# Kernel optimization log

Hardware: AMD Instinct MI355X
Metric: run time of the kernel (lower is better)

## Reference

```python
import jax, jax.numpy as jnp
import numpy as np

B, N, E = 64, 512, 524288
DA, DE, DH, DR, DI = 70, 14, 200, 16, 6
T_SCALE = float(np.sqrt(1.0 / 200.0))
D_MIN, D_MAX, D_COUNT = 0.0, 5.0, 16


def _layernorm(x, g, b, eps=1e-5):
    m = jnp.mean(x, axis=-1, keepdims=True)
    v = jnp.var(x, axis=-1, keepdims=True)
    return g * (x - m) * jax.lax.rsqrt(v + eps) + b


def setup_inputs() -> dict:
    key = jax.random.key(0)
    ks = jax.random.split(key, 24)
    d = {
        'atom_feat1': jax.random.normal(ks[0], (B, N, DA), jnp.float32),
        'atom_feat2': jax.random.normal(ks[1], (B, N, DA), jnp.float32),
        'coords1': jax.random.normal(ks[2], (B, N, 3), jnp.float32) * 3.0,
        'coords2': jax.random.normal(ks[3], (B, N, 3), jnp.float32) * 3.0,
        'edge_feat1': jax.random.normal(ks[4], (E, DE), jnp.float32),
        'edge_feat2': jax.random.normal(ks[5], (E, DE), jnp.float32),
        'interaction1': jax.random.normal(ks[6], (B, N, DI), jnp.float32),
        'interaction2': jax.random.normal(ks[7], (B, N, DI), jnp.float32),
        'edge_src1': jax.random.randint(ks[8], (E,), 0, B * N, jnp.int32),
        'edge_dst1': jax.random.randint(ks[9], (E,), 0, B * N, jnp.int32),
        'edge_src2': jax.random.randint(ks[10], (E,), 0, B * N, jnp.int32),
        'edge_dst2': jax.random.randint(ks[11], (E,), 0, B * N, jnp.int32),
        # parameters (scaled for stability)
        'W_atom': jax.random.normal(ks[12], (DA, DH), jnp.float32) * 0.1,
        'W_edge': jax.random.normal(ks[13], (DE, 100), jnp.float32) * 0.1,
        'W_rbf': jax.random.normal(ks[14], (D_COUNT, 100), jnp.float32) * 0.1,
        'b_rbf': jnp.zeros((100,), jnp.float32),
        'ln_g': jnp.ones((DH,), jnp.float32),
        'ln_b': jnp.zeros((DH,), jnp.float32),
        'W_down': jax.random.normal(ks[15], (2 * DH, DH), jnp.float32) * 0.05,
        'degree_table': jax.random.normal(ks[16], (200, DH), jnp.float32).at[0].set(0.0) * 0.1,
        'W_f1': jax.random.normal(ks[17], (3 * (DH + DI), 400), jnp.float32) * 0.05,
        'b_f1': jnp.zeros((400,), jnp.float32),
        'W_f2': jax.random.normal(ks[18], (400, 200), jnp.float32) * 0.05,
        'b_f2': jnp.zeros((200,), jnp.float32),
        'W_f3': jax.random.normal(ks[19], (200, 100), jnp.float32) * 0.05,
        'b_f3': jnp.zeros((100,), jnp.float32),
        'W_f4': jax.random.normal(ks[20], (100, 1), jnp.float32) * 0.05,
        'b_f4': jnp.zeros((1,), jnp.float32),
    }
    return d


def _side(atom, coords, efeat, src, dst, W_atom, W_edge, W_rbf, b_rbf, ln_g, ln_b):
    # atom: [B,N,DA], coords: [B,N,3], efeat: [E,DE], src/dst: [E] flat node ids
    BN = B * N
    h = jax.nn.relu(jnp.einsum('bna,ad->bnd', atom, W_atom)).reshape(BN, DH)
    e = jax.nn.relu(efeat @ W_edge)                      # [E,100]
    cflat = coords.reshape(BN, 3)
    diff = cflat[src] - cflat[dst]                       # [E,3]
    dist = jnp.sqrt(jnp.sum(diff * diff, axis=-1) + 1e-12)
    mu = jnp.linspace(D_MIN, D_MAX, D_COUNT)             # [16]
    sigma = (D_MAX - D_MIN) / D_COUNT
    rbf = jnp.exp(-(((dist[:, None] - mu[None, :]) / sigma) ** 2))  # [E,16]
    r = jax.nn.relu(rbf @ W_rbf + b_rbf)                 # [E,100]
    eh = jnp.concatenate([e, r], axis=-1)                # [E,200]
    h = _layernorm(h, ln_g, ln_b)
    eh = _layernorm(eh, ln_g, ln_b)
    # one message-passing aggregation (encoder step): scatter edge msgs to dst
    h = h + jax.ops.segment_sum(eh, dst, num_segments=BN)
    deg = jax.ops.segment_sum(jnp.ones((E,), jnp.int32), dst, num_segments=BN)
    deg = jnp.clip(deg, 0, 199)                          # in_degrees -> embedding idx
    return h.reshape(B, N, DH), deg.reshape(B, N)


def reference(atom_feat1, atom_feat2, coords1, coords2, edge_feat1, edge_feat2,
              interaction1, interaction2, edge_src1, edge_dst1, edge_src2, edge_dst2,
              W_atom, W_edge, W_rbf, b_rbf, ln_g, ln_b, W_down, degree_table,
              W_f1, b_f1, W_f2, b_f2, W_f3, b_f3, W_f4, b_f4):
    h1, d1 = _side(atom_feat1, coords1, edge_feat1, edge_src1, edge_dst1,
                   W_atom, W_edge, W_rbf, b_rbf, ln_g, ln_b)
    h2, d2 = _side(atom_feat2, coords2, edge_feat2, edge_src2, edge_dst2,
                   W_atom, W_edge, W_rbf, b_rbf, ln_g, ln_b)
    # batched cross-attention (atom_cross_att), vectorized over B
    att = jnp.einsum('bnd,bmd->bnm', h1, h2) * T_SCALE   # [B,N,N]
    a2 = jax.nn.softmax(att, axis=-1)
    a1 = jax.nn.softmax(att, axis=-2)
    c1 = jnp.einsum('bnm,bmd->bnd', a2, h2)              # for_hg1
    c2 = jnp.einsum('bnm,bnd->bmd', a1, h1)              # for_hg2
    h1 = jax.nn.relu(jnp.einsum('bnk,kd->bnd', jnp.concatenate([h1, c1], -1), W_down))
    h2 = jax.nn.relu(jnp.einsum('bnk,kd->bnd', jnp.concatenate([h2, c2], -1), W_down))
    h1 = h1 + degree_table[d1]
    h2 = h2 + degree_table[d2]
    # readout: mean over nodes, concat mean interaction embedding
    hsg1 = jnp.concatenate([jnp.mean(h1, axis=1), jnp.mean(interaction1, axis=1)], -1)
    hsg2 = jnp.concatenate([jnp.mean(h2, axis=1), jnp.mean(interaction2, axis=1)], -1)
    x = jnp.concatenate([hsg1, hsg2, hsg1 - hsg2], axis=-1)  # [B, 3*(200+6)]
    x = jax.nn.relu(x @ W_f1 + b_f1)
    x = jax.nn.relu(x @ W_f2 + b_f2)
    x = jax.nn.relu(x @ W_f3 + b_f3)
    zk = x @ W_f4 + b_f4                                 # [B,1]
    return zk
```

## Files before the change

kernel.cpp:

```cpp
#include <hip/hip_runtime.h>
#include <cstddef>
#include <cstdint>

#define BB   64
#define NN   512
#define BN   (BB*NN)
#define HBN  16384
#define EE   524288
#define DA   70
#define DE   14
#define DH   200
#define DI   6
#define T_SCALE 0.07071067811865475f

typedef __attribute__((ext_vector_type(8))) short short8;
typedef __attribute__((ext_vector_type(4))) float f32x4;

__device__ __forceinline__ short f2bf(float x) {
    union { float f; unsigned u; } v; v.f = x;
    const unsigned r = v.u + 0x7FFFu + ((v.u >> 16) & 1u);
    return (short)(r >> 16);
}
__device__ __forceinline__ float bf2f(short s) {
    union { unsigned u; float f; } v;
    v.u = ((unsigned)(unsigned short)s) << 16;
    return v.f;
}

__device__ __forceinline__ float dpp16_sum(float x) {
    union { float f; int i; } a, b;
    a.f = x;
    b.i = __builtin_amdgcn_update_dpp(0, a.i, 0xB1, 0xF, 0xF, false); a.f += b.f;
    b.i = __builtin_amdgcn_update_dpp(0, a.i, 0x4E, 0xF, 0xF, false); a.f += b.f;
    b.i = __builtin_amdgcn_update_dpp(0, a.i, 0x141, 0xF, 0xF, false); a.f += b.f;
    b.i = __builtin_amdgcn_update_dpp(0, a.i, 0x140, 0xF, 0xF, false); a.f += b.f;
    return a.f;
}

__global__ __launch_bounds__(256) void prologue_kernel(
    const float* __restrict__ atom1, const float* __restrict__ atom2,
    const float* __restrict__ W_atom,
    const float* __restrict__ ln_g, const float* __restrict__ ln_b,
    float* __restrict__ h1, float* __restrict__ h2,
    const int* __restrict__ edst1, const int* __restrict__ edst2,
    int* __restrict__ deg1, int* __restrict__ deg2,
    int* __restrict__ rank1, int* __restrict__ rank2,
    const float* __restrict__ W_edge, const float* __restrict__ W_rbf,
    const float* __restrict__ b_rbf,
    short* __restrict__ WTH, short* __restrict__ WTL,
    short* __restrict__ featH1, short* __restrict__ featH2,
    const float* __restrict__ W_down,
    short* __restrict__ WbTH, short* __restrict__ WbTL)
{
    const int bid = blockIdx.x;
    const int tid = threadIdx.x;

    if (bid < 4096) {
        const int side = bid >> 11;
        const float* atom = side ? atom2 : atom1;
        float* h = side ? h2 : h1;
        const int node0 = (bid & 2047) * 16;

        __shared__ float arow[16][DA];
        __shared__ float vals[16][DH];

        for (int i = tid; i < 16*DA; i += 256) {
            const int n = i / DA, k = i % DA;
            arow[n][k] = atom[(size_t)(node0+n)*DA + k];
        }
        __syncthreads();

        if (tid < DH) {
            float a[16];
            #pragma unroll
            for (int n = 0; n < 16; n++) a[n] = 0.f;
            for (int k = 0; k < DA; k++) {
                const float w = W_atom[k*DH + tid];
                #pragma unroll
                for (int n = 0; n < 16; n++) a[n] += arow[n][k]*w;
            }
            #pragma unroll
            for (int n = 0; n < 16; n++) vals[n][tid] = fmaxf(a[n], 0.f);
        }
        __syncthreads();

        const int wv = tid >> 6, lane = tid & 63;
        #pragma unroll 1
        for (int rr = 0; rr < 4; rr++) {
            const int n = rr*4 + wv;
            float v0 = vals[n][lane];
            float v1 = vals[n][64+lane];
            float v2 = vals[n][128+lane];
            float v3 = (lane < 8) ? vals[n][192+lane] : 0.0f;
            float s  = v0+v1+v2+v3;
            float s2 = v0*v0+v1*v1+v2*v2+v3*v3;
            #pragma unroll
            for (int off = 1; off < 64; off <<= 1) {
                s  += __shfl_xor(s,  off, 64);
                s2 += __shfl_xor(s2, off, 64);
            }
            const float mean = s * (1.0f/DH);
            const float var  = s2 * (1.0f/DH) - mean*mean;
            const float rstd = rsqrtf(var + 1e-5f);
            const size_t base = (size_t)(node0+n)*DH;
            h[base + lane]       = ln_g[lane]     *(v0-mean)*rstd + ln_b[lane];
            h[base + 64 + lane]  = ln_g[64+lane]  *(v1-mean)*rstd + ln_b[64+lane];
            h[base + 128 + lane] = ln_g[128+lane] *(v2-mean)*rstd + ln_b[128+lane];
            if (lane < 8)
                h[base + 192 + lane] = ln_g[192+lane]*(v3-mean)*rstd + ln_b[192+lane];
        }
        return;
    }

    if (bid < 6144) {
        const int e = (bid - 4096)*256 + tid;
        rank1[e] = atomicAdd(&deg1[edst1[e]], 1);
        rank2[e] = atomicAdd(&deg2[edst2[e]], 1);
        return;
    }

    if (bid < 6508) {
        const int idx = (bid - 6144)*256 + tid;
        if (idx >= 208*448) return;
        const int c = idx / 448, kk = idx - c*448;
        float v = 0.f;
        if (c < 200) {
            if (kk < 200) v = W_down[(size_t)kk*DH + c];
            else if (kk >= 224 && kk < 424) v = W_down[(size_t)(200 + kk - 224)*DH + c];
        }
        const short hi = f2bf(v);
        WbTH[idx] = hi;
        WbTL[idx] = f2bf(v - bf2f(hi));
        return;
    }

    {
        const int pb = bid - 6508;
        if (pb >= 26) {
            short* f = (pb == 26) ? featH1 : featH2;
            f[(size_t)EE*32 + tid] = 0;
            f[(size_t)EE*32 + 256 + tid] = 0;
            return;
        }
        const int idx = pb*256 + tid;
        const int c = idx >> 5, k = idx & 31;
        float v = 0.f;
        if (c < 100) {
            if (k < 14) v = W_edge[k*100 + c];
        } else if (c < 200) {
            const int cc = c - 100;
            if (k >= 14 && k < 30) v = W_rbf[(k-14)*100 + cc];
            else if (k == 30) v = b_rbf[cc];
        }
        const short hi = f2bf(v);
        WTH[idx] = hi;
        WTL[idx] = f2bf(v - bf2f(hi));
    }
}

__global__ __launch_bounds__(1024) void scan_kernel(
    const int* __restrict__ deg1, const int* __restrict__ deg2,
    int* __restrict__ start1, int* __restrict__ start2)
{
    const int side = blockIdx.x;
    const int* deg   = side ? deg2 : deg1;
    int* start  = side ? start2 : start1;

    __shared__ int part[1024];
    const int t = threadIdx.x;
    const int base = t * 32;
    int local[32];
    int sum = 0;
    #pragma unroll
    for (int i = 0; i < 8; i++) {
        const int4 v = *(const int4*)&deg[base + i*4];
        local[4*i+0] = v.x; local[4*i+1] = v.y;
        local[4*i+2] = v.z; local[4*i+3] = v.w;
        sum += v.x + v.y + v.z + v.w;
    }
    part[t] = sum;
    __syncthreads();
    for (int off = 1; off < 1024; off <<= 1) {
        int v = (t >= off) ? part[t-off] : 0;
        __syncthreads();
        part[t] += v;
        __syncthreads();
    }
    int run = part[t] - sum;
    #pragma unroll
    for (int i = 0; i < 32; i++) {
        start[base+i] = run;
        run += local[i];
    }
    if (t == 1023) start[BN] = run;
}

__global__ __launch_bounds__(256) void featgen_kernel(
    const float* __restrict__ efeat1, const float* __restrict__ efeat2,
    const int* __restrict__ esrc1, const int* __restrict__ esrc2,
    const int* __restrict__ edst1, const int* __restrict__ edst2,
    const float* __restrict__ coords1, const float* __restrict__ coords2,
    const int* __restrict__ rank1, const int* __restrict__ rank2,
    const int* __restrict__ start1, const int* __restrict__ start2,
    short* __restrict__ featH1, short* __restrict__ featH2)
{
    const int side = blockIdx.y;
    const float* ef     = side ? efeat2  : efeat1;
    const int*   esrc   = side ? esrc2   : esrc1;
    const int*   edst   = side ? edst2   : edst1;
    const float* coords = side ? coords2 : coords1;
    const int*   rank   = side ? rank2   : rank1;
    const int*   start  = side ? start2  : start1;
    short* featH = side ? featH2 : featH1;

    const int e = blockIdx.x*256 + threadIdx.x;
    const int src = esrc[e], dst = edst[e];

    short f[32];
    #pragma unroll
    for (int k = 0; k < 14; k++) f[k] = f2bf(ef[(size_t)e*DE + k]);

    const float dx = coords[src*3+0] - coords[dst*3+0];
    const float dy = coords[src*3+1] - coords[dst*3+1];
    const float dz = coords[src*3+2] - coords[dst*3+2];
    const float dist = sqrtf(dx*dx + dy*dy + dz*dz + 1e-12f);
    #pragma unroll
    for (int k = 0; k < 16; k++) {
        const float t = 3.2f*dist - 1.0666666667f*(float)k;
        f[14+k] = f2bf(__expf(-t*t));
    }
    f[30] = f2bf(1.0f);
    f[31] = 0;

    const int slot = start[dst] + rank[e];
    short* out = featH + (size_t)slot*32;
    #pragma unroll
    for (int q = 0; q < 4; q++)
        *(short8*)&out[q*8] = *(short8*)&f[q*8];
}

__global__ __launch_bounds__(256, 2) void gather_mfma(
    const short* __restrict__ featH1, const short* __restrict__ featH2,
    const int* __restrict__ start1, const int* __restrict__ start2,
    const short* __restrict__ WTH, const short* __restrict__ WTL,
    const float* __restrict__ ln_g, const float* __restrict__ ln_b,
    float* __restrict__ h1, float* __restrict__ h2)
{
    __shared__ short sWH[208*40];
    __shared__ short sWL[208*40];
    __shared__ float plane[4][216];

    const int tid = threadIdx.x;
    const int wv = tid >> 6, lane = tid & 63;
    const int arow = lane & 15, aq = lane >> 4;

    for (int f = tid; f < 832; f += 256) {
        const int d = f >> 2, cc = (f & 3) * 8;
        *(short8*)&sWH[d*40 + cc] = *(const short8*)&WTH[f*8];
        *(short8*)&sWL[d*40 + cc] = *(const short8*)&WTL[f*8];
    }
    __syncthreads();

    const int side = blockIdx.y;
    const short* feat = side ? featH2 : featH1;
    const int*  start = side ? start2 : start1;
    float* h = side ? h2 : h1;

    const int c0 = blockIdx.x*16 + wv*4;

    const float g0 = ln_g[lane],      bb0 = ln_b[lane];
    const float g1 = ln_g[64+lane],   bb1 = ln_b[64+lane];
    const float g2 = ln_g[128+lane],  bb2 = ln_b[128+lane];
    const float g3 = (lane < 8) ? ln_g[192+lane] : 0.f;
    const float bb3 = (lane < 8) ? ln_b[192+lane] : 0.f;

    const int sidx = (lane < 5) ? lane : 4;
    const int sv = start[c0 + sidx];

    const int lb = arow*40 + aq*8;

    #pragma unroll 1
    for (int ni = 0; ni < 4; ni++) {
        const int st = __builtin_amdgcn_readlane(sv, ni);
        const int en = __builtin_amdgcn_readlane(sv, ni + 1);
        const int dg = en - st;
        const int node = c0 + ni;
        const size_t hbase = (size_t)node * DH;

        const float hv0 = h[hbase + lane];
        const float hv1 = h[hbase + 64 + lane];
        const float hv2 = h[hbase + 128 + lane];
        const float hv3 = (lane < 8) ? h[hbase + 192 + lane] : 0.f;

        float colacc[13];
        #pragma unroll
        for (int nt = 0; nt < 13; nt++) colacc[nt] = 0.f;
        float musum = 0.f;

        short8 aC = *(const short8*)&feat[(size_t)(st + arow)*32 + aq*8];

        for (int t0 = 0; t0 < dg; t0 += 16) {
            const short8 aN = *(const short8*)&feat[(size_t)(st + t0 + 16 + arow)*32 + aq*8];

            f32x4 acc[13];
            #pragma unroll
            for (int nt = 0; nt < 13; nt++) {
                const short8 whv = *(const short8*)&sWH[nt*640 + lb];
                const short8 wlv = *(const short8*)&sWL[nt*640 + lb];
                f32x4 z = (f32x4){0.f,0.f,0.f,0.f};
                z = __builtin_amdgcn_mfma_f32_16x16x32_bf16(aC, whv, z, 0, 0, 0);
                z = __builtin_amdgcn_mfma_f32_16x16x32_bf16(aC, wlv, z, 0, 0, 0);
                acc[nt] = z;
            }
            float sr[4] = {0.f,0.f,0.f,0.f}, s2r[4] = {0.f,0.f,0.f,0.f};
            #pragma unroll
            for (int nt = 0; nt < 13; nt++) {
                #pragma unroll
                for (int r = 0; r < 4; r++) {
                    const float v = fmaxf(acc[nt][r], 0.f);
                    acc[nt][r] = v;
                    sr[r] += v; s2r[r] += v*v;
                }
            }
            #pragma unroll
            for (int r = 0; r < 4; r++) {
                sr[r]  = dpp16_sum(sr[r]);
                s2r[r] = dpp16_sum(s2r[r]);
            }
            #pragma unroll
            for (int r = 0; r < 4; r++) {
                const bool valid = (t0 + aq*4 + r) < dg;
                const float mean = sr[r] * (1.0f/DH);
                const float var  = s2r[r] * (1.0f/DH) - mean*mean;
                const float rs   = rsqrtf(var + 1e-5f);
                const float rstd = valid ? rs : 0.f;
                musum += valid ? mean*rs : 0.f;
                #pragma unroll
                for (int nt = 0; nt < 13; nt++)
                    colacc[nt] += rstd*acc[nt][r];
            }
            aC = aN;
        }

        #pragma unroll
        for (int nt = 0; nt < 13; nt++) {
            colacc[nt] += __shfl_xor(colacc[nt], 16, 64);
            colacc[nt] += __shfl_xor(colacc[nt], 32, 64);
        }
        musum += __shfl_xor(musum, 16, 64);
        musum += __shfl_xor(musum, 32, 64);

        if (aq == 0) {
            #pragma unroll
            for (int nt = 0; nt < 13; nt++)
                plane[wv][nt*16 + arow] = colacc[nt];
        }

        const float dgf = (float)dg;
        h[hbase + lane]       = hv0 + g0*(plane[wv][lane]     - musum) + dgf*bb0;
        h[hbase + 64 + lane]  = hv1 + g1*(plane[wv][64+lane]  - musum) + dgf*bb1;
        h[hbase + 128 + lane] = hv2 + g2*(plane[wv][128+lane] - musum) + dgf*bb2;
        if (lane < 8)
            h[hbase + 192 + lane] = hv3 + g3*(plane[wv][192+lane] - musum) + dgf*bb3;
    }
}

__global__ __launch_bounds__(256) void cvt_kernel(
    const float* __restrict__ h1, const float* __restrict__ h2, const int half,
    short* __restrict__ hbH1, short* __restrict__ hbL1,
    short* __restrict__ hbH2, short* __restrict__ hbL2,
    short* __restrict__ hTH1, short* __restrict__ hTL1,
    short* __restrict__ hTH2, short* __restrict__ hTL2)
{
    const int side = blockIdx.y;
    const float* h = side ? h2 : h1;
    short* hbH = side ? hbH2 : hbH1;
    short* hbL = side ? hbL2 : hbL1;
    short* hTH = side ? hTH2 : hTH1;
    short* hTL = side ? hTL2 : hTL1;

    const int nl0 = blockIdx.x * 64;
    const int bl = nl0 >> 9, m0 = nl0 & 511;
    const int ng0 = half*HBN + nl0;

    __shared__ short tH[64][226];
    __shared__ short tL[64][226];
    const int tid = threadIdx.x;
    for (int i = tid; i < 64*224; i += 256) {
        const int r = i / 224, c = i - r*224;
        const float v = (c < DH) ? h[(size_t)(ng0+r)*DH + c] : 0.f;
        const short hi = f2bf(v);
        const short lo = f2bf(v - bf2f(hi));
        tH[r][c] = hi; tL[r][c] = lo;
        hbH[(size_t)(nl0+r)*224 + c] = hi;
        hbL[(size_t)(nl0+r)*224 + c] = lo;
    }
    __syncthreads();
    for (int i = tid; i < 224*64; i += 256) {
        const int c = i >> 6, m = i & 63;
        const size_t o = ((size_t)bl*224 + c)*NN + m0 + m;
        hTH[o] = tH[m][c];
        hTL[o] = tL[m][c];
    }
}

__global__ __launch_bounds__(512, 2) void attn_kernel(
    const short* __restrict__ hbH1, const short* __restrict__ hbL1,
    const short* __restrict__ hbH2, const short* __restrict__ hbL2,
    const short* __restrict__ hTH1, const short* __restrict__ hTL1,
    const short* __restrict__ hTH2, const short* __restrict__ hTL2,
    short* __restrict__ cb1, short* __restrict__ cb2)
{
    const int id  = blockIdx.x;
    const int xcd = id & 7, m = id >> 3;
    const int r   = m >> 6;
    const int b01 = (m >> 5) & 1;
    const int dir = (m >> 4) & 1;
    const int qb  = m & 15;
    const int b   = xcd*4 + r*2 + b01;
    const int q0  = qb << 5;

    const short *Qh, *Ql, *Kh, *Kl, *Vh, *Vl;
    short* cb;
    if (dir == 0) {
        Qh = hbH1 + (size_t)b*NN*224;  Ql = hbL1 + (size_t)b*NN*224;
        Kh = hbH2 + (size_t)b*NN*224;  Kl = hbL2 + (size_t)b*NN*224;
        Vh = hTH2 + (size_t)b*224*NN;  Vl = hTL2 + (size_t)b*224*NN;
        cb = cb1;
    } else {
        Qh = hbH2 + (size_t)b*NN*224;  Ql = hbL2 + (size_t)b*NN*224;
        Kh = hbH1 + (size_t)b*NN*224;  Kl = hbL1 + (size_t)b*NN*224;
        Vh = hTH1 + (size_t)b*224*NN;  Vl = hTL1 + (size_t)b*224*NN;
        cb = cb2;
    }

    __shared__ short smem[32*520];
    short* sQh = smem;
    short* sQl = smem + 7424;
    short* pb  = smem;
    __shared__ float sm_[8][32];
    __shared__ float ss_[8][32];

    const int tid = threadIdx.x;
    const int wv = tid >> 6, lane = tid & 63;
    const int arow = lane & 15, aq = lane >> 4;

    for (int i = tid; i < 896; i += 512) {
        const int rr = i / 28, c = (i - rr*28) * 8;
        *(short8*)&sQh[rr*232 + c] = *(const short8*)&Qh[(size_t)(q0 + rr)*224 + c];
        *(short8*)&sQl[rr*232 + c] = *(const short8*)&Ql[(size_t)(q0 + rr)*224 + c];
    }
    __syncthreads();

    f32x4 acc[2][4];
    #pragma unroll
    for (int g = 0; g < 2; g++)
        #pragma unroll
        for (int t = 0; t < 4; t++) acc[g][t] = (f32x4){0.f,0.f,0.f,0.f};

    const int qb_off = arow*232 + aq*8;
    #pragma unroll 1
    for (int k = 0; k < 7; k++) {
        const short8 qh0 = *(const short8*)&sQh[qb_off + k*32];
        const short8 ql0 = *(const short8*)&sQl[qb_off + k*32];
        const short8 qh1 = *(const short8*)&sQh[qb_off + 16*232 + k*32];
        const short8 ql1 = *(const short8*)&sQl[qb_off + 16*232 + k*32];
        #pragma unroll
        for (int t = 0; t < 4; t++) {
            const size_t kb = (size_t)((wv*4 + t)*16 + arow)*224 + k*32 + aq*8;
            const short8 bh = *(const short8*)&Kh[kb];
            const short8 bl = *(const short8*)&Kl[kb];
            acc[0][t] = __builtin_amdgcn_mfma_f32_16x16x32_bf16(qh0, bh, acc[0][t], 0, 0, 0);
            acc[0][t] = __builtin_amdgcn_mfma_f32_16x16x32_bf16(qh0, bl, acc[0][t], 0, 0, 0);
            acc[0][t] = __builtin_amdgcn_mfma_f32_16x16x32_bf16(ql0, bh, acc[0][t], 0, 0, 0);
            acc[1][t] = __builtin_amdgcn_mfma_f32_16x16x32_bf16(qh1, bh, acc[1][t], 0, 0, 0);
            acc[1][t] = __builtin_amdgcn_mfma_f32_16x16x32_bf16(qh1, bl, acc[1][t], 0, 0, 0);
            acc[1][t] = __builtin_amdgcn_mfma_f32_16x16x32_bf16(ql1, bh, acc[1][t], 0, 0, 0);
        }
    }

    float iv[2][4];
    #pragma unroll
    for (int g = 0; g < 2; g++) {
        #pragma unroll
        for (int r2 = 0; r2 < 4; r2++) {
            float mx = -1e30f;
            #pragma unroll
            for (int t = 0; t < 4; t++) {
                acc[g][t][r2] *= T_SCALE;
                mx = fmaxf(mx, acc[g][t][r2]);
            }
            mx = fmaxf(mx, __shfl_xor(mx, 1, 64));
            mx = fmaxf(mx, __shfl_xor(mx, 2, 64));
            mx = fmaxf(mx, __shfl_xor(mx, 4, 64));
            mx = fmaxf(mx, __shfl_xor(mx, 8, 64));
            if (arow == 0) sm_[wv][g*16 + aq*4 + r2] = mx;
        }
    }
    __syncthreads();
    #pragma unroll
    for (int g = 0; g < 2; g++) {
        #pragma unroll
        for (int r2 = 0; r2 < 4; r2++) {
            const int row = g*16 + aq*4 + r2;
            float M = sm_[0][row];
            #pragma unroll
            for (int w = 1; w < 8; w++) M = fmaxf(M, sm_[w][row]);
            float s = 0.f;
            #pragma unroll
            for (int t = 0; t < 4; t++) {
                const float e = __expf(acc[g][t][r2] - M);
                acc[g][t][r2] = e;
                s += e;
            }
            s += __shfl_xor(s, 1, 64);
            s += __shfl_xor(s, 2, 64);
            s += __shfl_xor(s, 4, 64);
            s += __shfl_xor(s, 8, 64);
            if (arow == 0) ss_[wv][row] = s;
        }
    }
    __syncthreads();
    #pragma unroll
    for (int g = 0; g < 2; g++) {
        #pragma unroll
        for (int r2 = 0; r2 < 4; r2++) {
            const int row = g*16 + aq*4 + r2;
            float s = ss_[0][row];
            #pragma unroll
            for (int w = 1; w < 8; w++) s += ss_[w][row];
            iv[g][r2] = 1.0f / s;
        }
    }
    #pragma unroll
    for (int g = 0; g < 2; g++) {
        #pragma unroll
        for (int t = 0; t < 4; t++) {
            const int col = (wv*4 + t)*16 + arow;
            #pragma unroll
            for (int r2 = 0; r2 < 4; r2++)
                pb[(g*16 + aq*4 + r2)*520 + col] = f2bf(acc[g][t][r2] * iv[g][r2]);
        }
    }
    __syncthreads();

    const int nbase = (wv < 5) ? 2*wv : 10 + (wv - 5);
    const int ncnt  = (wv < 5) ? 2 : 1;
    f32x4 pacc[2][2];
    #pragma unroll
    for (int g = 0; g < 2; g++)
        #pragma unroll
        for (int t = 0; t < 2; t++) pacc[g][t] = (f32x4){0.f,0.f,0.f,0.f};

    for (int k0 = 0; k0 < NN; k0 += 32) {
        const short8 a0 = *(const short8*)&pb[arow*520 + k0 + aq*8];
        const short8 a1 = *(const short8*)&pb[(16 + arow)*520 + k0 + aq*8];
        #pragma unroll
        for (int t = 0; t < 2; t++) {
            if (t < ncnt) {
                const size_t vb = (size_t)((nbase+t)*16 + arow)*NN + k0 + aq*8;
                const short8 bh = *(const short8*)&Vh[vb];
                const short8 bl = *(const short8*)&Vl[vb];
                pacc[0][t] = __builtin_amdgcn_mfma_f32_16x16x32_bf16(a0, bh, pacc[0][t], 0, 0, 0);
                pacc[0][t] = __builtin_amdgcn_mfma_f32_16x16x32_bf16(a0, bl, pacc[0][t], 0, 0, 0);
                pacc[1][t] = __builtin_amdgcn_mfma_f32_16x16x32_bf16(a1, bh, pacc[1][t], 0, 0, 0);
                pacc[1][t] = __builtin_amdgcn_mfma_f32_16x16x32_bf16(a1, bl, pacc[1][t], 0, 0, 0);
            }
        }
    }

    #pragma unroll
    for (int t = 0; t < 2; t++) {
        if (t < ncnt) {
            const int col = (nbase+t)*16 + arow;
            #pragma unroll
            for (int g = 0; g < 2; g++) {
                #pragma unroll
                for (int r2 = 0; r2 < 4; r2++) {
                    const int row = q0 + g*16 + aq*4 + r2;
                    const short v = (col < DH) ? f2bf(pacc[g][t][r2]) : (short)0;
                    cb[((size_t)b*NN + row)*224 + col] = v;
                }
            }
        }
    }
    if (wv == 7) {
        const int col = 208 + arow;
        #pragma unroll
        for (int g = 0; g < 2; g++) {
            #pragma unroll
            for (int r2 = 0; r2 < 4; r2++) {
                const int row = q0 + g*16 + aq*4 + r2;
                cb[((size_t)b*NN + row)*224 + col] = 0;
            }
        }
    }
}

__global__ __launch_bounds__(512, 2) void down_mfma(
    const short* __restrict__ hbH1, const short* __restrict__ hbH2,
    const short* __restrict__ cb1, const short* __restrict__ cb2,
    const int* __restrict__ deg1, const int* __restrict__ deg2,
    const short* __restrict__ WbTH, const short* __restrict__ WbTL,
    const float* __restrict__ degree_table,
    float* __restrict__ hsg1, float* __restrict__ hsg2, const int half)
{
    const int side = blockIdx.y;
    const short* X0 = side ? hbH2 : hbH1;
    const short* X1 = side ? cb2 : cb1;
    const int*   dgp = side ? deg2 : deg1;
    float* hsg = side ? hsg2 : hsg1;

    const int nl0 = blockIdx.x * 128;
    const int ng0 = half*HBN + nl0;
    const int b = ng0 >> 9;

    __shared__ short As[128*40];
    __shared__ short BsH[208*40];
    __shared__ short BsL[208*40];
    __shared__ float part[208];

    const int tid = threadIdx.x;
    const int wv = tid >> 6, lane = tid & 63;
    const int arow = lane & 15, aq = lane >> 4;

    if (tid < 208) part[tid] = 0.f;

    f32x4 acc[13];
    #pragma unroll
    for (int t = 0; t < 13; t++) acc[t] = (f32x4){0.f,0.f,0.f,0.f};

    const int sr = tid >> 2, sc = (tid & 3) * 8;

    for (int phase = 0; phase < 2; phase++) {
        const short* X = phase ? X1 : X0;
        for (int k0 = 0; k0 < 224; k0 += 32) {
            __syncthreads();
            *(short8*)&As[sr*40 + sc] =
                *(const short8*)&X[(size_t)(nl0+sr)*224 + k0 + sc];
            const int kkg = phase*224 + k0;
            #pragma unroll
            for (int pass = 0; pass < 2; pass++) {
                const int f = pass*512 + tid;
                if (f < 832) {
                    const int d = f >> 2, cc = (f & 3) * 8;
                    *(short8*)&BsH[d*40 + cc] = *(const short8*)&WbTH[(size_t)d*448 + kkg + cc];
                    *(short8*)&BsL[d*40 + cc] = *(const short8*)&WbTL[(size_t)d*448 + kkg + cc];
                }
            }
            __syncthreads();
            const short8 a = *(const short8*)&As[(16*wv + arow)*40 + aq*8];
            #pragma unroll
            for (int t = 0; t < 13; t++) {
                const short8 bh = *(const short8*)&BsH[(t*16 + arow)*40 + aq*8];
                const short8 bl = *(const short8*)&BsL[(t*16 + arow)*40 + aq*8];
                acc[t] = __builtin_amdgcn_mfma_f32_16x16x32_bf16(a, bh, acc[t], 0, 0, 0);
                acc[t] = __builtin_amdgcn_mfma_f32_16x16x32_bf16(a, bl, acc[t], 0, 0, 0);
            }
        }
    }
    __syncthreads();

    int dgc[4];
    #pragma unroll
    for (int r = 0; r < 4; r++) {
        int d = dgp[ng0 + 16*wv + aq*4 + r];
        dgc[r] = d > 199 ? 199 : d;
    }
    #pragma unroll
    for (int nt = 0; nt < 13; nt++) {
        const int col = nt*16 + arow;
        float s = 0.f;
        if (col < DH) {
            #pragma unroll
            for (int r = 0; r < 4; r++)
                s += fmaxf(acc[nt][r], 0.f) + degree_table[dgc[r]*DH + col];
        }
        s += __shfl_xor(s, 16, 64);
        s += __shfl_xor(s, 32, 64);
        if (lane < 16 && col < DH) atomicAdd(&part[col], s);
    }
    __syncthreads();
    if (tid < DH) unsafeAtomicAdd(&hsg[b*206 + tid], part[tid] * (1.0f/512.0f));
}

__global__ __launch_bounds__(256) void mlp_kernel(
    const float* __restrict__ hsg1, const float* __restrict__ hsg2,
    const float* __restrict__ i1, const float* __restrict__ i2,
    const float* __restrict__ W_f1, const float* __restrict__ b_f1,
    const float* __restrict__ W_f2, const float* __restrict__ b_f2,
    const float* __restrict__ W_f3, const float* __restrict__ b_f3,
    const float* __restrict__ W_f4, const float* __restrict__ b_f4,
    float* __restrict__ out)
{
    const int b = blockIdx.x;
    __shared__ float x[618];
    __shared__ float y1[400];
    __shared__ float y2[200];
    __shared__ float y3[100];
    __shared__ float red[256];
    const int tid = threadIdx.x;

    if (tid < 192) {
        const int j = tid % 6, seg = tid / 6;
        float s1 = 0.f, s2 = 0.f;
        for (int n = seg*16; n < seg*16 + 16; n++) {
            s1 += i1[(size_t)b*NN*DI + n*DI + j];
            s2 += i2[(size_t)b*NN*DI + n*DI + j];
        }
        red[tid] = s1;
        y2[tid] = s2;
    }
    __syncthreads();
    if (tid < 206) {
        float a, bb;
        if (tid < 200) {
            a = hsg1[b*206 + tid]; bb = hsg2[b*206 + tid];
        } else {
            const int j = tid - 200;
            float t1 = 0.f, t2 = 0.f;
            for (int sg = 0; sg < 32; sg++) { t1 += red[sg*6 + j]; t2 += y2[sg*6 + j]; }
            a = t1 * (1.0f/512.0f); bb = t2 * (1.0f/512.0f);
        }
        x[tid] = a; x[206 + tid] = bb; x[412 + tid] = a - bb;
    }
    __syncthreads();
    for (int c = tid; c < 400; c += 256) {
        float acc = b_f1[c];
        for (int k = 0; k < 618; k++) acc += x[k]*W_f1[(size_t)k*400 + c];
        y1[c] = fmaxf(acc, 0.0f);
    }
    __syncthreads();
    if (tid < 200) {
        float acc = b_f2[tid];
        for (int k = 0; k < 400; k++) acc += y1[k]*W_f2[k*200 + tid];
        y2[tid] = fmaxf(acc, 0.0f);
    }
    __syncthreads();
    if (tid < 100) {
        float acc = b_f3[tid];
        for (int k = 0; k < 200; k++) acc += y2[k]*W_f3[k*100 + tid];
        y3[tid] = fmaxf(acc, 0.0f);
    }
    __syncthreads();
    red[tid] = (tid < 100) ? y3[tid]*W_f4[tid] : 0.0f;
    __syncthreads();
    for (int s = 128; s > 0; s >>= 1) {
        if (tid < s) red[tid] += red[tid + s];
        __syncthreads();
    }
    if (tid == 0) out[b] = red[0] + b_f4[0];
}

extern "C" void kernel_launch(void* const* d_in, const int* in_sizes, int n_in,
                              void* d_out, int out_size, void* d_ws, size_t ws_size,
                              hipStream_t stream)
{
    const float* atom1  = (const float*)d_in[0];
    const float* atom2  = (const float*)d_in[1];
    const float* coords1= (const float*)d_in[2];
    const float* coords2= (const float*)d_in[3];
    const float* efeat1 = (const float*)d_in[4];
    const float* efeat2 = (const float*)d_in[5];
    const float* inter1 = (const float*)d_in[6];
    const float* inter2 = (const float*)d_in[7];
    const int*   esrc1  = (const int*)d_in[8];
    const int*   edst1  = (const int*)d_in[9];
    const int*   esrc2  = (const int*)d_in[10];
    const int*   edst2  = (const int*)d_in[11];
    const float* W_atom = (const float*)d_in[12];
    const float* W_edge = (const float*)d_in[13];
    const float* W_rbf  = (const float*)d_in[14];
    const float* b_rbf  = (const float*)d_in[15];
    const float* ln_g   = (const float*)d_in[16];
    const float* ln_b   = (const float*)d_in[17];
    const float* W_down = (const float*)d_in[18];
    const float* deg_tab= (const float*)d_in[19];
    const float* W_f1   = (const float*)d_in[20];
    const float* b_f1   = (const float*)d_in[21];
    const float* W_f2   = (const float*)d_in[22];
    const float* b_f2   = (const float*)d_in[23];
    const float* W_f3   = (const float*)d_in[24];
    const float* b_f3   = (const float*)d_in[25];
    const float* W_f4   = (const float*)d_in[26];
    const float* b_f4   = (const float*)d_in[27];
    float* out = (float*)d_out;

    float* ws = (float*)d_ws;
    const size_t HSZ = (size_t)BN*DH;
    float* h1  = ws;
    float* h2  = h1 + HSZ;
    short* pool = (short*)(h2 + HSZ);
    const size_t FSZ = (size_t)(EE+16)*32;
    short* featH1 = pool;
    short* featH2 = featH1 + FSZ;
    const size_t HB = (size_t)32*NN*224;
    short* hbH1 = pool;           short* hbL1 = hbH1 + HB;
    short* hbH2 = hbL1 + HB;      short* hbL2 = hbH2 + HB;
    short* hTH1 = hbL2 + HB;      short* hTL1 = hTH1 + HB;
    short* hTH2 = hTL1 + HB;      short* hTL2 = hTH2 + HB;
    short* cb1  = hTL2 + HB;      short* cb2  = cb1 + HB;
    size_t pool_sz = 2*FSZ > 10*HB ? 2*FSZ : 10*HB;
    short* after = pool + pool_sz;
    short* WTH = after;
    short* WTL = WTH + 208*32;
    short* WbTH = WTL + 208*32;
    short* WbTL = WbTH + 208*448;
    float* hsg1 = (float*)(WbTL + 208*448);
    float* hsg2 = hsg1 + (size_t)BB*206;
    int* deg1 = (int*)(hsg2 + (size_t)BB*206);
    int* deg2 = deg1 + BN;
    int* start1 = deg2 + BN;
    int* start2 = start1 + (BN+1);
    int* cursor1 = start2 + (BN+1);
    int* cursor2 = cursor1 + BN;
    int* rank1 = cursor2 + BN;
    int* rank2 = rank1 + EE;

    hipMemsetAsync(deg1, 0, 2*(size_t)BN*sizeof(int), stream);
    hipMemsetAsync(hsg1, 0, 2*(size_t)BB*206*sizeof(float), stream);

    prologue_kernel<<<6536, 256, 0, stream>>>(
        atom1, atom2, W_atom, ln_g, ln_b, h1, h2,
        edst1, edst2, deg1, deg2, rank1, rank2,
        W_edge, W_rbf, b_rbf, WTH, WTL, featH1, featH2,
        W_down, WbTH, WbTL);

    scan_kernel<<<2, 1024, 0, stream>>>(deg1, deg2, start1, start2);

    featgen_kernel<<<dim3(EE/256, 2), 256, 0, stream>>>(
        efeat1, efeat2, esrc1, esrc2, edst1, edst2, coords1, coords2,
        rank1, rank2, start1, start2, featH1, featH2);

    gather_mfma<<<dim3(BN/16, 2), 256, 0, stream>>>(
        featH1, featH2, start1, start2, WTH, WTL, ln_g, ln_b, h1, h2);

    for (int half = 0; half < 2; half++) {
        cvt_kernel<<<dim3(HBN/64, 2), 256, 0, stream>>>(
            h1, h2, half, hbH1, hbL1, hbH2, hbL2, hTH1, hTL1, hTH2, hTL2);
        attn_kernel<<<1024, 512, 0, stream>>>(
            hbH1, hbL1, hbH2, hbL2, hTH1, hTL1, hTH2, hTL2, cb1, cb2);
        down_mfma<<<dim3(HBN/128, 2), 512, 0, stream>>>(
            hbH1, hbH2, cb1, cb2, deg1, deg2, WbTH, WbTL, deg_tab,
            hsg1, hsg2, half);
    }

    mlp_kernel<<<BB, 256, 0, stream>>>(
        hsg1, hsg2, inter1, inter2,
        W_f1, b_f1, W_f2, b_f2, W_f3, b_f3, W_f4, b_f4, out);
}
```

Measured before the change: 891.1 us.

## Double attention query tile to 64 rows per block to reuse K/V loads

Each attention block now handles 64 query rows instead of 32, so the grid halves from 1024 to 512 blocks and every K and V fragment loaded from global memory feeds four MFMA row groups instead of two. The goal is to halve redundant global K/V traffic per query row. In exchange the accumulator register count doubles and shared memory per block doubles to about 66KB. That may lower occupancy below the two blocks per CU the launch bounds request, and it leaves fewer blocks to fill the CUs.

```diff
diff --git a/kernel.cpp b/kernel.cpp
--- a/kernel.cpp
+++ b/kernel.cpp
@@ -413,12 +413,11 @@
 {
     const int id  = blockIdx.x;
     const int xcd = id & 7, m = id >> 3;
-    const int r   = m >> 6;
-    const int b01 = (m >> 5) & 1;
-    const int dir = (m >> 4) & 1;
-    const int qb  = m & 15;
-    const int b   = xcd*4 + r*2 + b01;
-    const int q0  = qb << 5;
+    const int b2  = m >> 4;
+    const int dir = (m >> 3) & 1;
+    const int qb  = m & 7;
+    const int b   = xcd*4 + b2;
+    const int q0  = qb << 6;
 
     const short *Qh, *Ql, *Kh, *Kl, *Vh, *Vl;
     short* cb;
@@ -434,54 +433,55 @@
         cb = cb2;
     }
 
-    __shared__ short smem[32*520];
+    __shared__ short smem[64*520];
     short* sQh = smem;
-    short* sQl = smem + 7424;
+    short* sQl = smem + 14848;
     short* pb  = smem;
-    __shared__ float sm_[8][32];
-    __shared__ float ss_[8][32];
+    __shared__ float sm_[8][64];
+    __shared__ float ss_[8][64];
 
     const int tid = threadIdx.x;
     const int wv = tid >> 6, lane = tid & 63;
     const int arow = lane & 15, aq = lane >> 4;
 
-    for (int i = tid; i < 896; i += 512) {
+    for (int i = tid; i < 1792; i += 512) {
         const int rr = i / 28, c = (i - rr*28) * 8;
         *(short8*)&sQh[rr*232 + c] = *(const short8*)&Qh[(size_t)(q0 + rr)*224 + c];
         *(short8*)&sQl[rr*232 + c] = *(const short8*)&Ql[(size_t)(q0 + rr)*224 + c];
     }
     __syncthreads();
 
-    f32x4 acc[2][4];
-    #pragma unroll
-    for (int g = 0; g < 2; g++)
+    f32x4 acc[4][4];
+    #pragma unroll
+    for (int g = 0; g < 4; g++)
         #pragma unroll
         for (int t = 0; t < 4; t++) acc[g][t] = (f32x4){0.f,0.f,0.f,0.f};
 
     const int qb_off = arow*232 + aq*8;
     #pragma unroll 1
     for (int k = 0; k < 7; k++) {
-        const short8 qh0 = *(const short8*)&sQh[qb_off + k*32];
-        const short8 ql0 = *(const short8*)&sQl[qb_off + k*32];
-        const short8 qh1 = *(const short8*)&sQh[qb_off + 16*232 + k*32];
-        const short8 ql1 = *(const short8*)&sQl[qb_off + 16*232 + k*32];
+        short8 qh[4], ql[4];
+        #pragma unroll
+        for (int g = 0; g < 4; g++) {
+            qh[g] = *(const short8*)&sQh[qb_off + g*16*232 + k*32];
+            ql[g] = *(const short8*)&sQl[qb_off + g*16*232 + k*32];
+        }
         #pragma unroll
         for (int t = 0; t < 4; t++) {
             const size_t kb = (size_t)((wv*4 + t)*16 + arow)*224 + k*32 + aq*8;
             const short8 bh = *(const short8*)&Kh[kb];
             const short8 bl = *(const short8*)&Kl[kb];
-            acc[0][t] = __builtin_amdgcn_mfma_f32_16x16x32_bf16(qh0, bh, acc[0][t], 0, 0, 0);
-            acc[0][t] = __builtin_amdgcn_mfma_f32_16x16x32_bf16(qh0, bl, acc[0][t], 0, 0, 0);
-            acc[0][t] = __builtin_amdgcn_mfma_f32_16x16x32_bf16(ql0, bh, acc[0][t], 0, 0, 0);
-            acc[1][t] = __builtin_amdgcn_mfma_f32_16x16x32_bf16(qh1, bh, acc[1][t], 0, 0, 0);
-            acc[1][t] = __builtin_amdgcn_mfma_f32_16x16x32_bf16(qh1, bl, acc[1][t], 0, 0, 0);
-            acc[1][t] = __builtin_amdgcn_mfma_f32_16x16x32_bf16(ql1, bh, acc[1][t], 0, 0, 0);
-        }
-    }
-
-    float iv[2][4];
-    #pragma unroll
-    for (int g = 0; g < 2; g++) {
+            #pragma unroll
+            for (int g = 0; g < 4; g++) {
+                acc[g][t] = __builtin_amdgcn_mfma_f32_16x16x32_bf16(qh[g], bh, acc[g][t], 0, 0, 0);
+                acc[g][t] = __builtin_amdgcn_mfma_f32_16x16x32_bf16(qh[g], bl, acc[g][t], 0, 0, 0);
+                acc[g][t] = __builtin_amdgcn_mfma_f32_16x16x32_bf16(ql[g], bh, acc[g][t], 0, 0, 0);
+            }
+        }
+    }
+
+    #pragma unroll
+    for (int g = 0; g < 4; g++) {
         #pragma unroll
         for (int r2 = 0; r2 < 4; r2++) {
             float mx = -1e30f;
@@ -499,7 +499,7 @@
     }
     __syncthreads();
     #pragma unroll
-    for (int g = 0; g < 2; g++) {
+    for (int g = 0; g < 4; g++) {
         #pragma unroll
         for (int r2 = 0; r2 < 4; r2++) {
             const int row = g*16 + aq*4 + r2;
@@ -522,49 +522,47 @@
     }
     __syncthreads();
     #pragma unroll
-    for (int g = 0; g < 2; g++) {
+    for (int g = 0; g < 4; g++) {
         #pragma unroll
         for (int r2 = 0; r2 < 4; r2++) {
             const int row = g*16 + aq*4 + r2;
             float s = ss_[0][row];
             #pragma unroll
             for (int w = 1; w < 8; w++) s += ss_[w][row];
-            iv[g][r2] = 1.0f / s;
-        }
-    }
-    #pragma unroll
-    for (int g = 0; g < 2; g++) {
-        #pragma unroll
-        for (int t = 0; t < 4; t++) {
-            const int col = (wv*4 + t)*16 + arow;
-            #pragma unroll
-            for (int r2 = 0; r2 < 4; r2++)
-                pb[(g*16 + aq*4 + r2)*520 + col] = f2bf(acc[g][t][r2] * iv[g][r2]);
+            const float iv = 1.0f / s;
+            #pragma unroll
+            for (int t = 0; t < 4; t++) {
+                const int col = (wv*4 + t)*16 + arow;
+                pb[row*520 + col] = f2bf(acc[g][t][r2] * iv);
+            }
         }
     }
     __syncthreads();
 
     const int nbase = (wv < 5) ? 2*wv : 10 + (wv - 5);
     const int ncnt  = (wv < 5) ? 2 : 1;
-    f32x4 pacc[2][2];
-    #pragma unroll
-    for (int g = 0; g < 2; g++)
+    f32x4 pacc[4][2];
+    #pragma unroll
+    for (int g = 0; g < 4; g++)
         #pragma unroll
         for (int t = 0; t < 2; t++) pacc[g][t] = (f32x4){0.f,0.f,0.f,0.f};
 
     for (int k0 = 0; k0 < NN; k0 += 32) {
-        const short8 a0 = *(const short8*)&pb[arow*520 + k0 + aq*8];
-        const short8 a1 = *(const short8*)&pb[(16 + arow)*520 + k0 + aq*8];
+        short8 a[4];
+        #pragma unroll
+        for (int g = 0; g < 4; g++)
+            a[g] = *(const short8*)&pb[(g*16 + arow)*520 + k0 + aq*8];
         #pragma unroll
         for (int t = 0; t < 2; t++) {
             if (t < ncnt) {
                 const size_t vb = (size_t)((nbase+t)*16 + arow)*NN + k0 + aq*8;
                 const short8 bh = *(const short8*)&Vh[vb];
                 const short8 bl = *(const short8*)&Vl[vb];
-                pacc[0][t] = __builtin_amdgcn_mfma_f32_16x16x32_bf16(a0, bh, pacc[0][t], 0, 0, 0);
-                pacc[0][t] = __builtin_amdgcn_mfma_f32_16x16x32_bf16(a0, bl, pacc[0][t], 0, 0, 0);
-                pacc[1][t] = __builtin_amdgcn_mfma_f32_16x16x32_bf16(a1, bh, pacc[1][t], 0, 0, 0);
-                pacc[1][t] = __builtin_amdgcn_mfma_f32_16x16x32_bf16(a1, bl, pacc[1][t], 0, 0, 0);
+                #pragma unroll
+                for (int g = 0; g < 4; g++) {
+                    pacc[g][t] = __builtin_amdgcn_mfma_f32_16x16x32_bf16(a[g], bh, pacc[g][t], 0, 0, 0);
+                    pacc[g][t] = __builtin_amdgcn_mfma_f32_16x16x32_bf16(a[g], bl, pacc[g][t], 0, 0, 0);
+                }
             }
         }
     }
@@ -574,7 +572,7 @@
         if (t < ncnt) {
             const int col = (nbase+t)*16 + arow;
             #pragma unroll
-            for (int g = 0; g < 2; g++) {
+            for (int g = 0; g < 4; g++) {
                 #pragma unroll
                 for (int r2 = 0; r2 < 4; r2++) {
                     const int row = q0 + g*16 + aq*4 + r2;
@@ -587,7 +585,7 @@
     if (wv == 7) {
         const int col = 208 + arow;
         #pragma unroll
-        for (int g = 0; g < 2; g++) {
+        for (int g = 0; g < 4; g++) {
             #pragma unroll
             for (int r2 = 0; r2 < 4; r2++) {
                 const int row = q0 + g*16 + aq*4 + r2;
@@ -838,7 +836,7 @@
     for (int half = 0; half < 2; half++) {
         cvt_kernel<<<dim3(HBN/64, 2), 256, 0, stream>>>(
             h1, h2, half, hbH1, hbL1, hbH2, hbL2, hTH1, hTL1, hTH2, hTL2);
-        attn_kernel<<<1024, 512, 0, stream>>>(
+        attn_kernel<<<512, 512, 0, stream>>>(
             hbH1, hbL1, hbH2, hbL2, hTH1, hTL1, hTH2, hTL2, cb1, cb2);
         down_mfma<<<dim3(HBN/128, 2), 512, 0, stream>>>(
             hbH1, hbH2, cb1, cb2, deg1, deg2, WbTH, WbTL, deg_tab,
```

Result: faster. 833.1 us (-6.5%).
